# Optimization experiments

Hardware: AMD Instinct MI355X
Metric: run time of the kernel (lower is better)

## Reference

```python
import jax, jax.numpy as jnp
import numpy as np

B = 32768
INPUT_DIM = 512
H_DIM = 512


def setup_inputs() -> dict:
    key = jax.random.key(0)
    ks = jax.random.split(key, 16)
    stdv = 1.0 / np.sqrt(H_DIM)
    def u(k, shape):
        return jax.random.uniform(k, shape, jnp.float32, -stdv, stdv)
    d_in = INPUT_DIM + H_DIM
    return {
        "x": jax.random.normal(ks[0], (B, INPUT_DIM), jnp.float32),
        "h": jax.random.normal(ks[1], (B, H_DIM), jnp.float32),
        "c": jax.random.normal(ks[2], (B, H_DIM), jnp.float32),
        "C": jax.random.normal(ks[3], (B, H_DIM), jnp.float32),
        "W_i": u(ks[4], (d_in, H_DIM)), "b_i": u(ks[5], (H_DIM,)),
        "W_f": u(ks[6], (d_in, H_DIM)), "b_f": u(ks[7], (H_DIM,)),
        "W_o": u(ks[8], (d_in, H_DIM)), "b_o": u(ks[9], (H_DIM,)),
        "W_g1": u(ks[10], (d_in, H_DIM)), "b_g1": u(ks[11], (H_DIM,)),
        "W_g2": u(ks[12], (d_in, H_DIM)), "b_g2": u(ks[13], (H_DIM,)),
        "W_mlp": u(ks[14], (2 * H_DIM, H_DIM)), "b_mlp": u(ks[15], (H_DIM,)),
    }


def reference(x, h, c, C, W_i, b_i, W_f, b_f, W_o, b_o, W_g1, b_g1, W_g2, b_g2, W_mlp, b_mlp):
    xh = jnp.concatenate([x, h], axis=1)  # [B, input_dim + h_dim]
    # Fuse the 5 gate GEMMs into one by concatenating weights along output dim.
    W_all = jnp.concatenate([W_i, W_f, W_o, W_g1, W_g2], axis=1)  # [d_in, 5*h]
    b_all = jnp.concatenate([b_i, b_f, b_o, b_g1, b_g2])
    gates = xh @ W_all + b_all  # [B, 5*h]
    zi, zf, zo, zg1, zg2 = jnp.split(gates, 5, axis=1)
    i = jax.nn.sigmoid(zi)
    f = jax.nn.sigmoid(zf)
    o = jax.nn.sigmoid(zo)
    g1 = jnp.tanh(zg1)
    g2 = jnp.tanh(zg2)
    new_c = f * c + i * g1
    new_C = f * C + i * g2
    cc = jnp.concatenate([new_c, new_C], axis=1)  # [B, 2*h]
    new_h = o * jnp.tanh(cc @ W_mlp + b_mlp)
    return new_h, new_c, new_C
```

## Files before the change

kernel.cpp:

```cpp
#include <hip/hip_runtime.h>
#include <hip/hip_bf16.h>

#define BROWS 32768
#define HDIM 512
#define DIN 1024
#define HB ((size_t)BROWS * HDIM)

typedef __attribute__((ext_vector_type(8))) __bf16 bf16x8;
typedef __attribute__((ext_vector_type(4))) float f32x4;
typedef __attribute__((ext_vector_type(8))) unsigned short us8;

__device__ inline unsigned short f2bf(float f) {
    union { float f; unsigned u; } v; v.f = f;
    unsigned r = v.u + 0x7fff + ((v.u >> 16) & 1);
    return (unsigned short)(r >> 16);
}
__device__ inline float bf2f(unsigned short b) {
    union { unsigned u; float f; } v; v.u = ((unsigned)b) << 16;
    return v.f;
}
__device__ inline float sigm(float z) { return 1.0f / (1.0f + __expf(-z)); }
__device__ inline float tanhfast(float z) { return 1.0f - 2.0f / (__expf(2.0f * z) + 1.0f); }

__device__ inline void gload_lds16(const void* gp, void* lp) {
    __builtin_amdgcn_global_load_lds((const __attribute__((address_space(1))) void*)gp,
                                     (__attribute__((address_space(3))) void*)lp, 16, 0, 0);
}

__global__ void cvt_xh(const float* __restrict__ x, const float* __restrict__ h,
                       unsigned short* __restrict__ xh) {
    const size_t total8 = (size_t)BROWS * DIN / 8;
    size_t stride = (size_t)gridDim.x * blockDim.x;
    for (size_t i = (size_t)blockIdx.x * blockDim.x + threadIdx.x; i < total8; i += stride) {
        size_t e = i * 8;
        size_t r = e >> 10;
        int k = (int)(e & 1023);
        const float* s = (k < HDIM) ? (x + r * HDIM + k) : (h + r * HDIM + (k - HDIM));
        f32x4 a = *(const f32x4*)s;
        f32x4 b = *(const f32x4*)(s + 4);
        us8 o;
        o[0] = f2bf(a[0]); o[1] = f2bf(a[1]); o[2] = f2bf(a[2]); o[3] = f2bf(a[3]);
        o[4] = f2bf(b[0]); o[5] = f2bf(b[1]); o[6] = f2bf(b[2]); o[7] = f2bf(b[3]);
        *(us8*)(xh + e) = o;
    }
}

struct WP { const float* w[6]; };

__global__ void wtrans(WP p, unsigned short* __restrict__ wt) {
    __shared__ float tile[64][65];
    const float* src = p.w[blockIdx.z];
    unsigned short* dst = wt + ((size_t)blockIdx.z << 19);
    int n0 = blockIdx.x * 64, k0 = blockIdx.y * 64;
    int t = threadIdx.x, r = t >> 2, q = t & 3;
    const float* s = src + (size_t)(k0 + r) * HDIM + n0 + q * 16;
#pragma unroll
    for (int j = 0; j < 16; j += 4) {
        f32x4 v = *(const f32x4*)(s + j);
        tile[r][q * 16 + j + 0] = v[0];
        tile[r][q * 16 + j + 1] = v[1];
        tile[r][q * 16 + j + 2] = v[2];
        tile[r][q * 16 + j + 3] = v[3];
    }
    __syncthreads();
    us8 o0, o1;
#pragma unroll
    for (int j = 0; j < 8; ++j) o0[j] = f2bf(tile[q * 16 + j][r]);
#pragma unroll
    for (int j = 0; j < 8; ++j) o1[j] = f2bf(tile[q * 16 + 8 + j][r]);
    unsigned short* d = dst + (size_t)(n0 + r) * DIN + k0 + q * 16;
    *(us8*)d = o0;
    *(us8*)(d + 8) = o1;
}

__global__ __launch_bounds__(256) void gemm_gates(
    const unsigned short* __restrict__ xh, const unsigned short* __restrict__ wt,
    const float* __restrict__ bi, const float* __restrict__ bf_,
    const float* __restrict__ bo, const float* __restrict__ bg1,
    const float* __restrict__ bg2,
    const float* __restrict__ cin, const float* __restrict__ Cin,
    float* __restrict__ out, unsigned short* __restrict__ obuf) {
    __shared__ __align__(16) unsigned short As[128][64];
    __shared__ __align__(16) unsigned short Bs[5][32][64];

    int bid = blockIdx.x;
    int wg = (bid & 7) * 512 + (bid >> 3);
    int mb = wg >> 4, nb = wg & 15;
    int r0 = mb * 128;
    int n0 = nb * 32;
    int t = threadIdx.x;
    int wv = t >> 6, lane = t & 63;
    int wr = wv >> 1, wc = wv & 1;

    f32x4 acc[5][4] = {};

    for (int kt = 0; kt < DIN / 64; ++kt) {
        int k0 = kt * 64;
#pragma unroll
        for (int i = 0; i < 4; ++i) {
            int ci = wv * 4 + i;
            int row = ci * 8 + (lane >> 3);
            int kc = (lane & 7) ^ (row & 7);
            const unsigned short* gp = xh + (size_t)(r0 + row) * DIN + k0 + kc * 8;
            gload_lds16(gp, &As[ci * 8][0]);
        }
#pragma unroll
        for (int i = 0; i < 5; ++i) {
            int q = wv * 5 + i;
            int g = q >> 2, rb = q & 3;
            int row = rb * 8 + (lane >> 3);
            int kc = (lane & 7) ^ (row & 7);
            const unsigned short* gp = wt + ((size_t)g << 19) + (size_t)(n0 + row) * DIN + k0 + kc * 8;
            gload_lds16(gp, &Bs[g][rb * 8][0]);
        }
        __syncthreads();
#pragma unroll
        for (int kk = 0; kk < 2; ++kk) {
            bf16x8 a[4];
#pragma unroll
            for (int m = 0; m < 4; ++m) {
                int row = wr * 64 + m * 16 + (lane & 15);
                int chunk = kk * 4 + (lane >> 4);
                int off = row * 128 + ((chunk ^ (row & 7)) << 4);
                a[m] = *(const bf16x8*)((const char*)&As[0][0] + off);
            }
#pragma unroll
            for (int g = 0; g < 5; ++g) {
                int row = wc * 16 + (lane & 15);
                int chunk = kk * 4 + (lane >> 4);
                int off = row * 128 + ((chunk ^ (row & 7)) << 4);
                bf16x8 b = *(const bf16x8*)((const char*)&Bs[g][0][0] + off);
#pragma unroll
                for (int m = 0; m < 4; ++m)
                    acc[g][m] = __builtin_amdgcn_mfma_f32_16x16x32_bf16(a[m], b, acc[g][m], 0, 0, 0);
            }
        }
        __syncthreads();
    }

    int cg = n0 + wc * 16 + (lane & 15);
    float vbi = bi[cg], vbf = bf_[cg], vbo = bo[cg], vbg1 = bg1[cg], vbg2 = bg2[cg];
#pragma unroll
    for (int m = 0; m < 4; ++m) {
        int rbase = r0 + wr * 64 + m * 16 + ((lane >> 4) << 2);
#pragma unroll
        for (int j = 0; j < 4; ++j) {
            size_t off = (size_t)(rbase + j) * HDIM + cg;
            float iv = sigm(acc[0][m][j] + vbi);
            float fv = sigm(acc[1][m][j] + vbf);
            float ov = sigm(acc[2][m][j] + vbo);
            float g1 = tanhfast(acc[3][m][j] + vbg1);
            float g2 = tanhfast(acc[4][m][j] + vbg2);
            float cell = cin[off], Cc = Cin[off];
            out[HB + off] = fv * cell + iv * g1;
            out[2 * HB + off] = fv * Cc + iv * g2;
            obuf[off] = f2bf(ov);
        }
    }
}

__global__ __launch_bounds__(256) void gemm_mlp(
    const float* __restrict__ outbase, const unsigned short* __restrict__ wtm,
    const float* __restrict__ bm, const unsigned short* __restrict__ obuf,
    float* __restrict__ out) {
    __shared__ __align__(16) unsigned short As[128][64];
    __shared__ __align__(16) unsigned short Bs[64][64];

    int bid = blockIdx.x;
    int wg = (bid & 7) * 256 + (bid >> 3);
    int mb = wg >> 3, nb = wg & 7;
    int r0 = mb * 128, n0 = nb * 64;
    int t = threadIdx.x, wv = t >> 6, lane = t & 63;
    int wr = wv >> 1, wc = wv & 1;

    f32x4 acc[4][2] = {};

    for (int kt = 0; kt < 16; ++kt) {
        int k0 = kt * 64;
        const float* asrc = (kt < 8) ? (outbase + HB) : (outbase + 2 * HB);
        int kcol = k0 & (HDIM - 1);
        {
            int row = t >> 1, half = t & 1;
            const float* s = asrc + (size_t)(r0 + row) * HDIM + kcol + half * 32;
            unsigned short tmp[32];
#pragma unroll
            for (int j = 0; j < 32; j += 4) {
                f32x4 v = *(const f32x4*)(s + j);
                tmp[j] = f2bf(v[0]); tmp[j + 1] = f2bf(v[1]);
                tmp[j + 2] = f2bf(v[2]); tmp[j + 3] = f2bf(v[3]);
            }
#pragma unroll
            for (int cj = 0; cj < 4; ++cj) {
                int chunk = half * 4 + cj;
                int off = row * 128 + ((chunk ^ (row & 7)) << 4);
                *(us8*)((char*)&As[0][0] + off) = *(const us8*)&tmp[cj * 8];
            }
        }
#pragma unroll
        for (int i = 0; i < 2; ++i) {
            int rb = wv * 2 + i;
            int row = rb * 8 + (lane >> 3);
            int kc = (lane & 7) ^ (row & 7);
            const unsigned short* gp = wtm + (size_t)(n0 + row) * DIN + k0 + kc * 8;
            gload_lds16(gp, &Bs[rb * 8][0]);
        }
        __syncthreads();
#pragma unroll
        for (int kk = 0; kk < 2; ++kk) {
            bf16x8 a[4];
#pragma unroll
            for (int m = 0; m < 4; ++m) {
                int row = wr * 64 + m * 16 + (lane & 15);
                int chunk = kk * 4 + (lane >> 4);
                int off = row * 128 + ((chunk ^ (row & 7)) << 4);
                a[m] = *(const bf16x8*)((const char*)&As[0][0] + off);
            }
#pragma unroll
            for (int n = 0; n < 2; ++n) {
                int row = wc * 32 + n * 16 + (lane & 15);
                int chunk = kk * 4 + (lane >> 4);
                int off = row * 128 + ((chunk ^ (row & 7)) << 4);
                bf16x8 b = *(const bf16x8*)((const char*)&Bs[0][0] + off);
#pragma unroll
                for (int m = 0; m < 4; ++m)
                    acc[m][n] = __builtin_amdgcn_mfma_f32_16x16x32_bf16(a[m], b, acc[m][n], 0, 0, 0);
            }
        }
        __syncthreads();
    }

#pragma unroll
    for (int n = 0; n < 2; ++n) {
        int cg = n0 + wc * 32 + n * 16 + (lane & 15);
        float vb = bm[cg];
#pragma unroll
        for (int m = 0; m < 4; ++m) {
            int rbase = r0 + wr * 64 + m * 16 + ((lane >> 4) << 2);
#pragma unroll
            for (int j = 0; j < 4; ++j) {
                size_t off = (size_t)(rbase + j) * HDIM + cg;
                float z = acc[m][n][j] + vb;
                out[off] = bf2f(obuf[off]) * tanhfast(z);
            }
        }
    }
}

extern "C" void kernel_launch(void* const* d_in, const int* in_sizes, int n_in,
                              void* d_out, int out_size, void* d_ws, size_t ws_size,
                              hipStream_t stream) {
    const float* x  = (const float*)d_in[0];
    const float* h  = (const float*)d_in[1];
    const float* c  = (const float*)d_in[2];
    const float* C  = (const float*)d_in[3];
    const float* Wi = (const float*)d_in[4];  const float* bi  = (const float*)d_in[5];
    const float* Wf = (const float*)d_in[6];  const float* bf  = (const float*)d_in[7];
    const float* Wo = (const float*)d_in[8];  const float* bo  = (const float*)d_in[9];
    const float* Wg1 = (const float*)d_in[10]; const float* bg1 = (const float*)d_in[11];
    const float* Wg2 = (const float*)d_in[12]; const float* bg2 = (const float*)d_in[13];
    const float* Wm = (const float*)d_in[14]; const float* bm  = (const float*)d_in[15];
    float* out = (float*)d_out;

    unsigned short* wt   = (unsigned short*)d_ws;
    unsigned short* xh   = wt + (6u << 19);
    unsigned short* obuf = xh + (size_t)BROWS * DIN;

    WP wp;
    wp.w[0] = Wi; wp.w[1] = Wf; wp.w[2] = Wo; wp.w[3] = Wg1; wp.w[4] = Wg2; wp.w[5] = Wm;

    cvt_xh<<<dim3(4096), dim3(256), 0, stream>>>(x, h, xh);
    wtrans<<<dim3(8, 16, 6), dim3(256), 0, stream>>>(wp, wt);
    gemm_gates<<<dim3(4096), dim3(256), 0, stream>>>(xh, wt, bi, bf, bo, bg1, bg2, c, C, out, obuf);
    gemm_mlp<<<dim3(2048), dim3(256), 0, stream>>>(out, wt + (5u << 19), bm, obuf, out);
}
```

Before: 785.6 us.

## Double-buffer LDS in both GEMMs and emit bf16 concat buffer for MLP

Both GEMM kernels get a two-stage LDS ping-pong: the tiles for step k+1 are loaded asynchronously while the MFMAs for step k run, and only one barrier is kept per iteration. The gates epilogue also writes new_c and new_C as bf16 into a concatenated [B,1024] workspace buffer. The MLP kernel can then stream its A operand straight into LDS with the direct global-to-LDS path instead of reading fp32 and converting it. This doubles LDS use per block, which may lower occupancy, and adds an extra bf16 write in the gates epilogue.

```diff
diff --git a/kernel.cpp b/kernel.cpp
--- a/kernel.cpp
+++ b/kernel.cpp
@@ -79,9 +79,10 @@
     const float* __restrict__ bo, const float* __restrict__ bg1,
     const float* __restrict__ bg2,
     const float* __restrict__ cin, const float* __restrict__ Cin,
-    float* __restrict__ out, unsigned short* __restrict__ obuf) {
-    __shared__ __align__(16) unsigned short As[128][64];
-    __shared__ __align__(16) unsigned short Bs[5][32][64];
+    float* __restrict__ out, unsigned short* __restrict__ obuf,
+    unsigned short* __restrict__ ccbuf) {
+    __shared__ __align__(16) unsigned short As[2][128][64];
+    __shared__ __align__(16) unsigned short Bs[2][5][32][64];
 
     int bid = blockIdx.x;
     int wg = (bid & 7) * 512 + (bid >> 3);
@@ -94,7 +95,7 @@
 
     f32x4 acc[5][4] = {};
 
-    for (int kt = 0; kt < DIN / 64; ++kt) {
+    auto stage = [&](int kt, int b) {
         int k0 = kt * 64;
 #pragma unroll
         for (int i = 0; i < 4; ++i) {
@@ -102,7 +103,7 @@
             int row = ci * 8 + (lane >> 3);
             int kc = (lane & 7) ^ (row & 7);
             const unsigned short* gp = xh + (size_t)(r0 + row) * DIN + k0 + kc * 8;
-            gload_lds16(gp, &As[ci * 8][0]);
+            gload_lds16(gp, &As[b][ci * 8][0]);
         }
 #pragma unroll
         for (int i = 0; i < 5; ++i) {
@@ -111,9 +112,16 @@
             int row = rb * 8 + (lane >> 3);
             int kc = (lane & 7) ^ (row & 7);
             const unsigned short* gp = wt + ((size_t)g << 19) + (size_t)(n0 + row) * DIN + k0 + kc * 8;
-            gload_lds16(gp, &Bs[g][rb * 8][0]);
-        }
-        __syncthreads();
+            gload_lds16(gp, &Bs[b][g][rb * 8][0]);
+        }
+    };
+
+    stage(0, 0);
+    __syncthreads();
+
+    int cur = 0;
+    for (int kt = 0; kt < DIN / 64; ++kt) {
+        if (kt < DIN / 64 - 1) stage(kt + 1, cur ^ 1);
 #pragma unroll
         for (int kk = 0; kk < 2; ++kk) {
             bf16x8 a[4];
@@ -122,20 +130,21 @@
                 int row = wr * 64 + m * 16 + (lane & 15);
                 int chunk = kk * 4 + (lane >> 4);
                 int off = row * 128 + ((chunk ^ (row & 7)) << 4);
-                a[m] = *(const bf16x8*)((const char*)&As[0][0] + off);
+                a[m] = *(const bf16x8*)((const char*)&As[cur][0][0] + off);
             }
 #pragma unroll
             for (int g = 0; g < 5; ++g) {
                 int row = wc * 16 + (lane & 15);
                 int chunk = kk * 4 + (lane >> 4);
                 int off = row * 128 + ((chunk ^ (row & 7)) << 4);
-                bf16x8 b = *(const bf16x8*)((const char*)&Bs[g][0][0] + off);
+                bf16x8 b = *(const bf16x8*)((const char*)&Bs[cur][g][0][0] + off);
 #pragma unroll
                 for (int m = 0; m < 4; ++m)
                     acc[g][m] = __builtin_amdgcn_mfma_f32_16x16x32_bf16(a[m], b, acc[g][m], 0, 0, 0);
             }
         }
         __syncthreads();
+        cur ^= 1;
     }
 
     int cg = n0 + wc * 16 + (lane & 15);
@@ -151,20 +160,24 @@
             float ov = sigm(acc[2][m][j] + vbo);
             float g1 = tanhfast(acc[3][m][j] + vbg1);
             float g2 = tanhfast(acc[4][m][j] + vbg2);
-            float cell = cin[off], Cc = Cin[off];
-            out[HB + off] = fv * cell + iv * g1;
-            out[2 * HB + off] = fv * Cc + iv * g2;
+            float ncv = fv * cin[off] + iv * g1;
+            float nCv = fv * Cin[off] + iv * g2;
+            out[HB + off] = ncv;
+            out[2 * HB + off] = nCv;
             obuf[off] = f2bf(ov);
+            size_t ccoff = (size_t)(rbase + j) * DIN + cg;
+            ccbuf[ccoff] = f2bf(ncv);
+            ccbuf[ccoff + HDIM] = f2bf(nCv);
         }
     }
 }
 
 __global__ __launch_bounds__(256) void gemm_mlp(
-    const float* __restrict__ outbase, const unsigned short* __restrict__ wtm,
+    const unsigned short* __restrict__ ccbuf, const unsigned short* __restrict__ wtm,
     const float* __restrict__ bm, const unsigned short* __restrict__ obuf,
     float* __restrict__ out) {
-    __shared__ __align__(16) unsigned short As[128][64];
-    __shared__ __align__(16) unsigned short Bs[64][64];
+    __shared__ __align__(16) unsigned short As[2][128][64];
+    __shared__ __align__(16) unsigned short Bs[2][64][64];
 
     int bid = blockIdx.x;
     int wg = (bid & 7) * 256 + (bid >> 3);
@@ -175,26 +188,15 @@
 
     f32x4 acc[4][2] = {};
 
-    for (int kt = 0; kt < 16; ++kt) {
+    auto stage = [&](int kt, int b) {
         int k0 = kt * 64;
-        const float* asrc = (kt < 8) ? (outbase + HB) : (outbase + 2 * HB);
-        int kcol = k0 & (HDIM - 1);
-        {
-            int row = t >> 1, half = t & 1;
-            const float* s = asrc + (size_t)(r0 + row) * HDIM + kcol + half * 32;
-            unsigned short tmp[32];
-#pragma unroll
-            for (int j = 0; j < 32; j += 4) {
-                f32x4 v = *(const f32x4*)(s + j);
-                tmp[j] = f2bf(v[0]); tmp[j + 1] = f2bf(v[1]);
-                tmp[j + 2] = f2bf(v[2]); tmp[j + 3] = f2bf(v[3]);
-            }
-#pragma unroll
-            for (int cj = 0; cj < 4; ++cj) {
-                int chunk = half * 4 + cj;
-                int off = row * 128 + ((chunk ^ (row & 7)) << 4);
-                *(us8*)((char*)&As[0][0] + off) = *(const us8*)&tmp[cj * 8];
-            }
+#pragma unroll
+        for (int i = 0; i < 4; ++i) {
+            int ci = wv * 4 + i;
+            int row = ci * 8 + (lane >> 3);
+            int kc = (lane & 7) ^ (row & 7);
+            const unsigned short* gp = ccbuf + (size_t)(r0 + row) * DIN + k0 + kc * 8;
+            gload_lds16(gp, &As[b][ci * 8][0]);
         }
 #pragma unroll
         for (int i = 0; i < 2; ++i) {
@@ -202,9 +204,16 @@
             int row = rb * 8 + (lane >> 3);
             int kc = (lane & 7) ^ (row & 7);
             const unsigned short* gp = wtm + (size_t)(n0 + row) * DIN + k0 + kc * 8;
-            gload_lds16(gp, &Bs[rb * 8][0]);
-        }
-        __syncthreads();
+            gload_lds16(gp, &Bs[b][rb * 8][0]);
+        }
+    };
+
+    stage(0, 0);
+    __syncthreads();
+
+    int cur = 0;
+    for (int kt = 0; kt < 16; ++kt) {
+        if (kt < 15) stage(kt + 1, cur ^ 1);
 #pragma unroll
         for (int kk = 0; kk < 2; ++kk) {
             bf16x8 a[4];
@@ -213,20 +222,21 @@
                 int row = wr * 64 + m * 16 + (lane & 15);
                 int chunk = kk * 4 + (lane >> 4);
                 int off = row * 128 + ((chunk ^ (row & 7)) << 4);
-                a[m] = *(const bf16x8*)((const char*)&As[0][0] + off);
+                a[m] = *(const bf16x8*)((const char*)&As[cur][0][0] + off);
             }
 #pragma unroll
             for (int n = 0; n < 2; ++n) {
                 int row = wc * 32 + n * 16 + (lane & 15);
                 int chunk = kk * 4 + (lane >> 4);
                 int off = row * 128 + ((chunk ^ (row & 7)) << 4);
-                bf16x8 b = *(const bf16x8*)((const char*)&Bs[0][0] + off);
+                bf16x8 b = *(const bf16x8*)((const char*)&Bs[cur][0][0] + off);
 #pragma unroll
                 for (int m = 0; m < 4; ++m)
                     acc[m][n] = __builtin_amdgcn_mfma_f32_16x16x32_bf16(a[m], b, acc[m][n], 0, 0, 0);
             }
         }
         __syncthreads();
+        cur ^= 1;
     }
 
 #pragma unroll
@@ -261,15 +271,16 @@
     const float* Wm = (const float*)d_in[14]; const float* bm  = (const float*)d_in[15];
     float* out = (float*)d_out;
 
-    unsigned short* wt   = (unsigned short*)d_ws;
-    unsigned short* xh   = wt + (6u << 19);
-    unsigned short* obuf = xh + (size_t)BROWS * DIN;
+    unsigned short* wt    = (unsigned short*)d_ws;
+    unsigned short* xh    = wt + (6u << 19);
+    unsigned short* obuf  = xh + (size_t)BROWS * DIN;
+    unsigned short* ccbuf = obuf + HB;
 
     WP wp;
     wp.w[0] = Wi; wp.w[1] = Wf; wp.w[2] = Wo; wp.w[3] = Wg1; wp.w[4] = Wg2; wp.w[5] = Wm;
 
     cvt_xh<<<dim3(4096), dim3(256), 0, stream>>>(x, h, xh);
     wtrans<<<dim3(8, 16, 6), dim3(256), 0, stream>>>(wp, wt);
-    gemm_gates<<<dim3(4096), dim3(256), 0, stream>>>(xh, wt, bi, bf, bo, bg1, bg2, c, C, out, obuf);
-    gemm_mlp<<<dim3(2048), dim3(256), 0, stream>>>(out, wt + (5u << 19), bm, obuf, out);
-}
+    gemm_gates<<<dim3(4096), dim3(256), 0, stream>>>(xh, wt, bi, bf, bo, bg1, bg2, c, C, out, obuf, ccbuf);
+    gemm_mlp<<<dim3(2048), dim3(256), 0, stream>>>(ccbuf, wt + (5u << 19), bm, obuf, out);
+}
```

After: 779.4 us. No clear change (-0.8%).
